# Kernel optimization log

Measured on AMD Instinct MI355X. Metric: run time of the kernel, lower is better.

The kernel has to match this reference:

```python
import jax, jax.numpy as jnp
import numpy as np

DM = 1024
N_HEADS = 16
DK = DM // N_HEADS
BS, SEQ = 4, 2048


def setup_inputs() -> dict:
    key = jax.random.key(0)
    k1, k2, k3 = jax.random.split(key, 3)
    scale = 1.0 / np.sqrt(DM)
    return {
        "x": jax.random.normal(k1, (BS, SEQ, DM), dtype=jnp.float32),
        "w_qkv": jax.random.normal(k2, (DM, 3 * DM), dtype=jnp.float32) * scale,
        "b_qkv": jnp.zeros((3 * DM,), dtype=jnp.float32),
        "w_out": jax.random.normal(k3, (DM, DM), dtype=jnp.float32) * scale,
        "b_out": jnp.zeros((DM,), dtype=jnp.float32),
    }


def reference(x, w_qkv, b_qkv, w_out, b_out):
    bs, seq_len, dm = x.shape
    qkv = x @ w_qkv + b_qkv                      # [bs, seq, 3*dm]
    q, k, v = jnp.split(qkv, 3, axis=-1)
    # [bs, heads, seq, dk]
    def heads(t):
        return t.reshape(bs, seq_len, N_HEADS, DK).transpose(0, 2, 1, 3)
    q, k, v = heads(q), heads(k), heads(v)
    w = jnp.einsum("bhqd,bhkd->bhqk", q, k) / np.sqrt(DK)
    causal = jnp.tril(jnp.ones((seq_len, seq_len), dtype=bool))
    w = jnp.where(causal, w, -jnp.inf)
    w = jax.nn.softmax(w, axis=-1)               # attn_dropout p=0 -> identity
    z = jnp.einsum("bhqk,bhkd->bhqd", w, v)
    z = z.transpose(0, 2, 1, 3).reshape(bs, seq_len, dm)
    return z @ w_out + b_out                     # resid_dropout p=0 -> identity
```

## Files before the change

kernel.cpp:

```cpp
#include <hip/hip_runtime.h>
#include <hip/hip_bf16.h>

typedef unsigned short u16;
typedef unsigned int u32;
typedef short bf16x8 __attribute__((ext_vector_type(8)));
typedef float f32x4 __attribute__((ext_vector_type(4)));

#define DM 1024
#define SEQ 2048
#define MTOK 8192
#define NQKV 3072

#define QSCALE 0.18033688011112042f

#define BAR() __builtin_amdgcn_s_barrier()
#define VMW(n) asm volatile("s_waitcnt vmcnt(" #n ")" ::: "memory")
#define LGKW() asm volatile("s_waitcnt lgkmcnt(0)" ::: "memory")

__device__ __forceinline__ u16 f2bf(float f) {
  union { float f; unsigned u; } a; a.f = f;
  unsigned r = a.u + 0x7FFFu + ((a.u >> 16) & 1u);
  return (u16)(r >> 16);
}

__device__ __forceinline__ u32 cvt2(float a, float b) {
  __hip_bfloat162 t = __float22bfloat162_rn(make_float2(a, b));
  u32 r; __builtin_memcpy(&r, &t, 4); return r;
}

__device__ __forceinline__ void gload_lds16(const u16* g, u16* l) {
  __builtin_amdgcn_global_load_lds(
      (const __attribute__((address_space(1))) unsigned int*)g,
      (__attribute__((address_space(3))) unsigned int*)l, 16, 0, 0);
}

__global__ __launch_bounds__(256) void cast_x_kernel(const float* __restrict__ in,
                                                     u16* __restrict__ out) {
  int i = blockIdx.x * 256 + threadIdx.x;
  float4 v = ((const float4*)in)[i];
  ushort4 o;
  o.x = f2bf(v.x); o.y = f2bf(v.y); o.z = f2bf(v.z); o.w = f2bf(v.w);
  ((ushort4*)out)[i] = o;
}

__global__ __launch_bounds__(256) void transpose_cast_kernel(const float* __restrict__ in,
                                                             u16* __restrict__ out,
                                                             int R, int C) {
  __shared__ float tile[32][33];
  const int tx = threadIdx.x & 31, ty = threadIdx.x >> 5;
  const int r0 = blockIdx.y << 5, c0 = blockIdx.x << 5;
#pragma unroll
  for (int i = 0; i < 32; i += 8)
    tile[ty + i][tx] = in[(size_t)(r0 + ty + i) * C + (c0 + tx)];
  __syncthreads();
#pragma unroll
  for (int i = 0; i < 32; i += 8)
    out[(size_t)(c0 + ty + i) * R + (r0 + tx)] = f2bf(tile[tx][ty + i]);
}

template <int EPI>
__global__ __launch_bounds__(256, 2) void gemm2_kernel(
    const u16* __restrict__ A, const u16* __restrict__ Bt,
    const float* __restrict__ bias,
    u16* __restrict__ oq, u16* __restrict__ ok, u16* __restrict__ ovT,
    float* __restrict__ of, int N) {
  __shared__ alignas(16) u16 As[2][128 * 64];
  __shared__ alignas(16) u16 Bs[2][128 * 64];

  const int tid = threadIdx.x, lane = tid & 63, wid = tid >> 6;
  const int wr = wid >> 1, wc = wid & 1;
  const int l15 = lane & 15, l4 = lane >> 4;
  const int swz = l15 & 7;

  const int xcd = blockIdx.x & 7, idx = blockIdx.x >> 3;
  const int row0 = ((xcd << 3) + (idx & 7)) << 7;
  const int col0 = (idx >> 3) << 7;

  const int sr = tid >> 3;
  const int scsw = ((tid & 7) ^ (sr & 7)) << 3;
  const u16* asrc = A + (size_t)(row0 + sr) * 1024 + scsw;
  const u16* bsrc = Bt + (size_t)(col0 + sr) * 1024 + scsw;

  auto stage = [&](int buf, int kt) {
#pragma unroll
    for (int j = 0; j < 4; ++j)
      gload_lds16(asrc + (size_t)(j << 5) * 1024 + (kt << 6),
                  &As[buf][0] + (j << 11) + tid * 8);
#pragma unroll
    for (int j = 0; j < 4; ++j)
      gload_lds16(bsrc + (size_t)(j << 5) * 1024 + (kt << 6),
                  &Bs[buf][0] + (j << 11) + tid * 8);
  };

  f32x4 acc[4][4];
#pragma unroll
  for (int m = 0; m < 4; ++m)
#pragma unroll
    for (int n = 0; n < 4; ++n) acc[m][n] = (f32x4){0.f, 0.f, 0.f, 0.f};

  stage(0, 0);
  stage(1, 1);

  int cur = 0;
#pragma unroll 1
  for (int t = 0; t < 16; ++t) {
    if (t < 15) { VMW(8); } else { VMW(0); }
    BAR();

    bf16x8 af[4][2], bfr[4][2];
    {
      const u16* base = &As[cur][0] + ((wr << 6) + l15) * 64;
#pragma unroll
      for (int mf = 0; mf < 4; ++mf)
#pragma unroll
        for (int ks = 0; ks < 2; ++ks)
          af[mf][ks] = *(const bf16x8*)(base + (mf << 4) * 64 + ((((ks << 2) + l4) ^ swz) << 3));
    }
    {
      const u16* base = &Bs[cur][0] + ((wc << 6) + l15) * 64;
#pragma unroll
      for (int nf = 0; nf < 4; ++nf)
#pragma unroll
        for (int ks = 0; ks < 2; ++ks)
          bfr[nf][ks] = *(const bf16x8*)(base + (nf << 4) * 64 + ((((ks << 2) + l4) ^ swz) << 3));
    }
    LGKW();
    BAR();
    if (t < 14) stage(cur, t + 2);

    __builtin_amdgcn_s_setprio(1);
#pragma unroll
    for (int ks = 0; ks < 2; ++ks)
#pragma unroll
      for (int mf = 0; mf < 4; ++mf)
#pragma unroll
        for (int nf = 0; nf < 4; ++nf)
          acc[mf][nf] = __builtin_amdgcn_mfma_f32_16x16x32_bf16(af[mf][ks], bfr[nf][ks],
                                                                acc[mf][nf], 0, 0, 0);
    __builtin_amdgcn_s_setprio(0);
    cur ^= 1;
  }

#pragma unroll
  for (int nf = 0; nf < 4; ++nf) {
    const int col = col0 + (wc << 6) + (nf << 4) + l15;
    const float bv = bias[col];
    if (EPI == 0) {
      const int sel = col >> 10;
      const int h = (col & 1023) >> 6;
      const int d = col & 63;
      const float scl = (sel == 0) ? QSCALE : 1.0f;
#pragma unroll
      for (int mf = 0; mf < 4; ++mf)
#pragma unroll
        for (int r = 0; r < 4; ++r) {
          const int row = row0 + (wr << 6) + (mf << 4) + (l4 << 2) + r;
          const int bb = row >> 11, s = row & 2047;
          const u16 v = f2bf((acc[mf][nf][r] + bv) * scl);
          const int bh = (bb << 4) + h;
          if (sel == 0)      oq[((size_t)bh * SEQ + s) * 64 + d] = v;
          else if (sel == 1) ok[((size_t)bh * SEQ + s) * 64 + d] = v;
          else               ovT[((size_t)bh * 64 + d) * SEQ + s] = v;
        }
    } else {
#pragma unroll
      for (int mf = 0; mf < 4; ++mf)
#pragma unroll
        for (int r = 0; r < 4; ++r) {
          const int row = row0 + (wr << 6) + (mf << 4) + (l4 << 2) + r;
          of[(size_t)row * N + col] = acc[mf][nf][r] + bv;
        }
    }
  }
}

__global__ __launch_bounds__(256, 4) void attn_kernel(const u16* __restrict__ qb,
                                                      const u16* __restrict__ kbuf,
                                                      const u16* __restrict__ vT,
                                                      u16* __restrict__ zb) {
  __shared__ alignas(16) u16 Ks[2][64 * 64];
  __shared__ alignas(16) u16 Vs[2][64 * 64];
  __shared__ alignas(16) u16 Ps[4][16 * 64];

  const int bid = blockIdx.x;
  const int xcd = bid & 7;
  const int idx = bid >> 3;
  const int bh = (xcd << 3) | (idx & 7);
  const int qpart = idx >> 3;
  const u32 qtab[4] = {0x0304080Fu, 0x0205090Eu, 0x01060A0Du, 0x00070B0Cu};
  const int qseg = (int)((qtab[qpart & 3] >> ((qpart >> 2) << 3)) & 15u);
  const int b = bh >> 4, h = bh & 15;

  const int tid = threadIdx.x;
  const int lane = tid & 63, wid = tid >> 6;
  const int l15 = lane & 15, l4 = lane >> 4;
  const int swz = l15 & 7;

  const u16* qp = qb + (size_t)bh * SEQ * 64;
  const u16* kp = kbuf + (size_t)bh * SEQ * 64;
  const u16* vp = vT + (size_t)bh * 64 * SEQ;

  const int qw0 = (qseg << 7) + (wid << 5);
  const int nkt = (qseg + 1) << 1;
  const int ktmax = (qseg << 1) + (wid >> 1);

  const int srow = tid >> 3;
  const int schk = ((tid & 7) ^ (srow & 7)) << 3;
  const u16* ksrc = kp + (size_t)srow * 64 + schk;
  const u16* vsrc = vp + (size_t)srow * SEQ + schk;

  auto stage = [&](int buf, int kt) {
    gload_lds16(ksrc + (size_t)kt * 4096, &Ks[buf][0] + tid * 8);
    gload_lds16(ksrc + (size_t)kt * 4096 + 32 * 64, &Ks[buf][0] + 2048 + tid * 8);
    gload_lds16(vsrc + (size_t)kt * 64, &Vs[buf][0] + tid * 8);
    gload_lds16(vsrc + (size_t)kt * 64 + (size_t)32 * SEQ, &Vs[buf][0] + 2048 + tid * 8);
  };

  bf16x8 aq[2][2];
#pragma unroll
  for (int m = 0; m < 2; ++m)
#pragma unroll
    for (int c = 0; c < 2; ++c)
      aq[m][c] = *(const bf16x8*)(qp + (size_t)(qw0 + (m << 4) + l15) * 64 + (c << 5) + (l4 << 3));
  asm volatile("" :: "v"(aq[0][0]), "v"(aq[0][1]), "v"(aq[1][0]), "v"(aq[1][1]));

  const short osv = (short)0x3F80;
  const bf16x8 onesf = {osv, osv, osv, osv, osv, osv, osv, osv};

  f32x4 zo[2][5];
  float mrun[2] = {-INFINITY, -INFINITY};
#pragma unroll
  for (int m = 0; m < 2; ++m)
#pragma unroll
    for (int d = 0; d < 5; ++d) zo[m][d] = (f32x4){0.f, 0.f, 0.f, 0.f};

  u16* pw = &Ps[wid][0];

  stage(0, 0);
  stage(1, 1);

  int cur = 0;
#pragma unroll 1
  for (int kt = 0; kt < nkt; ++kt) {
    if (kt + 1 < nkt) { VMW(4); } else { VMW(0); }
    BAR();

    if (kt <= ktmax) {
      const int k0 = kt << 6;
      const u16* kb_ = &Ks[cur][0];
      const u16* vb_ = &Vs[cur][0];
      f32x4 s[2][4];
#pragma unroll
      for (int m = 0; m < 2; ++m)
#pragma unroll
        for (int nf = 0; nf < 4; ++nf) s[m][nf] = (f32x4){0.f, 0.f, 0.f, 0.f};
#pragma unroll
      for (int nf = 0; nf < 4; ++nf) {
        const u16* kr = kb_ + ((nf << 4) + l15) * 64;
        const bf16x8 kf0 = *(const bf16x8*)(kr + ((l4 ^ swz) << 3));
        const bf16x8 kf1 = *(const bf16x8*)(kr + (((l4 + 4) ^ swz) << 3));
#pragma unroll
        for (int m = 0; m < 2; ++m) {
          s[m][nf] = __builtin_amdgcn_mfma_f32_16x16x32_bf16(kf0, aq[m][0], s[m][nf], 0, 0, 0);
          s[m][nf] = __builtin_amdgcn_mfma_f32_16x16x32_bf16(kf1, aq[m][1], s[m][nf], 0, 0, 0);
        }
      }
      if (kt == ktmax) {
#pragma unroll
        for (int m = 0; m < 2; ++m) {
          const int qtok = qw0 + (m << 4) + l15;
#pragma unroll
          for (int nf = 0; nf < 4; ++nf)
#pragma unroll
            for (int r = 0; r < 4; ++r) {
              const int ktok = k0 + (nf << 4) + (l4 << 2) + r;
              if (ktok > qtok) s[m][nf][r] = -INFINITY;
            }
        }
      }
      bf16x8 pa[2][2];
#pragma unroll
      for (int m = 0; m < 2; ++m) {
        float mx = s[m][0][0];
#pragma unroll
        for (int nf = 0; nf < 4; ++nf)
#pragma unroll
          for (int r = 0; r < 4; ++r) mx = fmaxf(mx, s[m][nf][r]);
        mx = fmaxf(mx, __shfl_xor(mx, 16));
        mx = fmaxf(mx, __shfl_xor(mx, 32));
        if (__ballot(mx > mrun[m])) {
          const float mnew = fmaxf(mrun[m], mx);
          const float alpha = exp2f(mrun[m] - mnew);
          mrun[m] = mnew;
#pragma unroll
          for (int d = 0; d < 5; ++d) zo[m][d] *= alpha;
        }
#pragma unroll
        for (int nf = 0; nf < 4; ++nf) {
          f32x4 p;
#pragma unroll
          for (int r = 0; r < 4; ++r) p[r] = exp2f(s[m][nf][r] - mrun[m]);
          const int phys = ((nf << 1) + (l4 >> 1)) ^ swz;
          uint2 o; o.x = cvt2(p[0], p[1]); o.y = cvt2(p[2], p[3]);
          *(uint2*)(pw + l15 * 64 + phys * 8 + ((l4 & 1) << 2)) = o;
        }
#pragma unroll
        for (int c = 0; c < 2; ++c) {
          const int phys = ((c << 2) + l4) ^ swz;
          pa[m][c] = *(const bf16x8*)(pw + l15 * 64 + phys * 8);
        }
      }
#pragma unroll
      for (int d = 0; d < 4; ++d) {
        const u16* vr = vb_ + ((d << 4) + l15) * 64;
        const bf16x8 vf0 = *(const bf16x8*)(vr + ((l4 ^ swz) << 3));
        const bf16x8 vf1 = *(const bf16x8*)(vr + (((l4 + 4) ^ swz) << 3));
        zo[0][d] = __builtin_amdgcn_mfma_f32_16x16x32_bf16(vf0, pa[0][0], zo[0][d], 0, 0, 0);
        zo[0][d] = __builtin_amdgcn_mfma_f32_16x16x32_bf16(vf1, pa[0][1], zo[0][d], 0, 0, 0);
        zo[1][d] = __builtin_amdgcn_mfma_f32_16x16x32_bf16(vf0, pa[1][0], zo[1][d], 0, 0, 0);
        zo[1][d] = __builtin_amdgcn_mfma_f32_16x16x32_bf16(vf1, pa[1][1], zo[1][d], 0, 0, 0);
      }
      zo[0][4] = __builtin_amdgcn_mfma_f32_16x16x32_bf16(onesf, pa[0][0], zo[0][4], 0, 0, 0);
      zo[0][4] = __builtin_amdgcn_mfma_f32_16x16x32_bf16(onesf, pa[0][1], zo[0][4], 0, 0, 0);
      zo[1][4] = __builtin_amdgcn_mfma_f32_16x16x32_bf16(onesf, pa[1][0], zo[1][4], 0, 0, 0);
      zo[1][4] = __builtin_amdgcn_mfma_f32_16x16x32_bf16(onesf, pa[1][1], zo[1][4], 0, 0, 0);
    }

    BAR();
    if (kt + 2 < nkt) stage(cur, kt + 2);
    cur ^= 1;
  }

#pragma unroll
  for (int m = 0; m < 2; ++m) {
    const float inv = 1.0f / zo[m][4][0];
    const int q = qw0 + (m << 4) + l15;
#pragma unroll
    for (int d = 0; d < 4; ++d) {
      uint2 o;
      o.x = cvt2(zo[m][d][0] * inv, zo[m][d][1] * inv);
      o.y = cvt2(zo[m][d][2] * inv, zo[m][d][3] * inv);
      *(uint2*)(zb + (((size_t)b * SEQ + q) * 16 + h) * 64 + (d << 4) + (l4 << 2)) = o;
    }
  }
}

extern "C" void kernel_launch(void* const* d_in, const int* in_sizes, int n_in,
                              void* d_out, int out_size, void* d_ws, size_t ws_size,
                              hipStream_t stream) {
  const float* x     = (const float*)d_in[0];
  const float* w_qkv = (const float*)d_in[1];
  const float* b_qkv = (const float*)d_in[2];
  const float* w_out = (const float*)d_in[3];
  const float* b_out = (const float*)d_in[4];
  float* out = (float*)d_out;

  char* ws = (char*)d_ws;
  u16* xb    = (u16*)ws;  ws += (size_t)MTOK * DM * 2;
  u16* wqkvT = (u16*)ws;  ws += (size_t)NQKV * DM * 2;
  u16* woutT = (u16*)ws;  ws += (size_t)DM * DM * 2;
  u16* qb    = (u16*)ws;  ws += (size_t)MTOK * DM * 2;
  u16* kb    = (u16*)ws;  ws += (size_t)MTOK * DM * 2;
  u16* vTb   = (u16*)ws;  ws += (size_t)MTOK * DM * 2;
  u16* zbuf  = (u16*)ws;  ws += (size_t)MTOK * DM * 2;

  cast_x_kernel<<<MTOK * DM / 1024, 256, 0, stream>>>(x, xb);
  transpose_cast_kernel<<<dim3(NQKV / 32, DM / 32), 256, 0, stream>>>(w_qkv, wqkvT, DM, NQKV);
  transpose_cast_kernel<<<dim3(DM / 32, DM / 32), 256, 0, stream>>>(w_out, woutT, DM, DM);

  gemm2_kernel<0><<<1536, 256, 0, stream>>>(xb, wqkvT, b_qkv, qb, kb, vTb, nullptr, NQKV);

  attn_kernel<<<1024, 256, 0, stream>>>(qb, kb, vTb, zbuf);

  gemm2_kernel<1><<<512, 256, 0, stream>>>(zbuf, woutT, b_out, nullptr, nullptr, nullptr, out, DM);
}
```

Measured before the change: 192.3 us.

## Add 256x256-tile 8-wave QKV GEMM with split-stage pipelined loads

Replaces the 128x128-tile QKV projection GEMM with a dedicated 512-thread kernel that computes 256x256 tiles, one block per CU. Each K step loads its tile in two halves interleaved with four quadrant MFMA phases, so global-to-LDS staging overlaps compute. The larger tile raises arithmetic intensity and cuts redundant global loads. In exchange it uses 128KB of LDS and 128 accumulator registers per thread, and the grid shrinks to 384 blocks, which risks wave-quantization imbalance across CUs. The output GEMM is de-templated, with no functional change.

```diff
diff --git a/kernel.cpp b/kernel.cpp
--- a/kernel.cpp
+++ b/kernel.cpp
@@ -58,12 +58,128 @@
     out[(size_t)(c0 + ty + i) * R + (r0 + tx)] = f2bf(tile[tx][ty + i]);
 }
 
-template <int EPI>
+__global__ __launch_bounds__(512, 1) void gemm8_qkv_kernel(
+    const u16* __restrict__ A, const u16* __restrict__ Bt,
+    const float* __restrict__ bias,
+    u16* __restrict__ oq, u16* __restrict__ ok, u16* __restrict__ ovT) {
+  __shared__ alignas(16) u16 As8[2][256 * 64];
+  __shared__ alignas(16) u16 Bs8[2][256 * 64];
+
+  const int tid = threadIdx.x, lane = tid & 63, wid = tid >> 6;
+  const int wm = wid >> 2, wn = wid & 3;
+  const int l15 = lane & 15, l4 = lane >> 4;
+  const int swz = l15 & 7;
+
+  const int bid = blockIdx.x;
+  const int xcd = bid & 7, i = bid >> 3;
+  const int brow = (xcd << 2) + (i & 3);
+  const int bcol = i >> 2;
+  const int row0 = brow << 8, col0 = bcol << 8;
+
+  const int sr = tid >> 3;
+  const int sc = tid & 7;
+
+  auto stageU = [&](int buf, int kt, int half) {
+#pragma unroll
+    for (int j = 0; j < 2; ++j) {
+      const int r = (half << 7) + (j << 6) + sr;
+      gload_lds16(Bt + (size_t)(col0 + r) * 1024 + (kt << 6) + ((sc ^ (r & 7)) << 3),
+                  &Bs8[buf][0] + r * 64 + (sc << 3));
+    }
+#pragma unroll
+    for (int j = 0; j < 2; ++j) {
+      const int r = (half << 7) + (j << 6) + sr;
+      gload_lds16(A + (size_t)(row0 + r) * 1024 + (kt << 6) + ((sc ^ (r & 7)) << 3),
+                  &As8[buf][0] + r * 64 + (sc << 3));
+    }
+  };
+
+  f32x4 acc[8][4];
+#pragma unroll
+  for (int m = 0; m < 8; ++m)
+#pragma unroll
+    for (int n = 0; n < 4; ++n) acc[m][n] = (f32x4){0.f, 0.f, 0.f, 0.f};
+
+  bf16x8 af[4][2], bf0[2][2], bf1[2][2];
+
+  auto rdA = [&](int buf, int mh) {
+    const u16* base = &As8[buf][0] + ((wm << 7) + (mh << 6) + l15) * 64;
+#pragma unroll
+    for (int mf = 0; mf < 4; ++mf)
+#pragma unroll
+      for (int ks = 0; ks < 2; ++ks)
+        af[mf][ks] = *(const bf16x8*)(base + (mf << 4) * 64 + ((((ks << 2) + l4) ^ swz) << 3));
+  };
+  auto rdB = [&](bf16x8 (&bf)[2][2], int buf, int nh) {
+    const u16* base = &Bs8[buf][0] + ((wn << 6) + (nh << 5) + l15) * 64;
+#pragma unroll
+    for (int nfl = 0; nfl < 2; ++nfl)
+#pragma unroll
+      for (int ks = 0; ks < 2; ++ks)
+        bf[nfl][ks] = *(const bf16x8*)(base + (nfl << 4) * 64 + ((((ks << 2) + l4) ^ swz) << 3));
+  };
+  auto mm = [&](bf16x8 (&bf)[2][2], int mh, int nh) {
+    __builtin_amdgcn_s_setprio(1);
+#pragma unroll
+    for (int mf = 0; mf < 4; ++mf)
+#pragma unroll
+      for (int nfl = 0; nfl < 2; ++nfl)
+#pragma unroll
+        for (int ks = 0; ks < 2; ++ks)
+          acc[(mh << 2) + mf][(nh << 1) + nfl] = __builtin_amdgcn_mfma_f32_16x16x32_bf16(
+              af[mf][ks], bf[nfl][ks], acc[(mh << 2) + mf][(nh << 1) + nfl], 0, 0, 0);
+    __builtin_amdgcn_s_setprio(0);
+  };
+
+  stageU(0, 0, 0);
+  stageU(0, 0, 1);
+
+#pragma unroll 1
+  for (int t = 0; t < 16; ++t) {
+    const int buf = t & 1, nbuf = buf ^ 1;
+    if (t < 15) { stageU(nbuf, t + 1, 0); VMW(4); } else { VMW(0); }
+    BAR();
+    rdA(buf, 0); rdB(bf0, buf, 0);
+    mm(bf0, 0, 0);
+    BAR();
+    if (t < 15) stageU(nbuf, t + 1, 1);
+    BAR();
+    rdB(bf1, buf, 1);
+    mm(bf1, 0, 1);
+    BAR();
+    rdA(buf, 1);
+    mm(bf0, 1, 0);
+    BAR();
+    mm(bf1, 1, 1);
+    BAR();
+  }
+
+#pragma unroll
+  for (int nf = 0; nf < 4; ++nf) {
+    const int col = col0 + (wn << 6) + (nf << 4) + l15;
+    const float bv = bias[col];
+    const int sel = col >> 10;
+    const int hh = (col & 1023) >> 6;
+    const int d = col & 63;
+    const float scl = (sel == 0) ? QSCALE : 1.0f;
+#pragma unroll
+    for (int mf = 0; mf < 8; ++mf)
+#pragma unroll
+      for (int r = 0; r < 4; ++r) {
+        const int row = row0 + (wm << 7) + (mf << 4) + (l4 << 2) + r;
+        const int bb = row >> 11, s = row & 2047;
+        const u16 v = f2bf((acc[mf][nf][r] + bv) * scl);
+        const int bh = (bb << 4) + hh;
+        if (sel == 0)      oq[((size_t)bh * SEQ + s) * 64 + d] = v;
+        else if (sel == 1) ok[((size_t)bh * SEQ + s) * 64 + d] = v;
+        else               ovT[((size_t)bh * 64 + d) * SEQ + s] = v;
+      }
+  }
+}
+
 __global__ __launch_bounds__(256, 2) void gemm2_kernel(
     const u16* __restrict__ A, const u16* __restrict__ Bt,
-    const float* __restrict__ bias,
-    u16* __restrict__ oq, u16* __restrict__ ok, u16* __restrict__ ovT,
-    float* __restrict__ of, int N) {
+    const float* __restrict__ bias, float* __restrict__ of, int N) {
   __shared__ alignas(16) u16 As[2][128 * 64];
   __shared__ alignas(16) u16 Bs[2][128 * 64];
 
@@ -145,32 +261,13 @@
   for (int nf = 0; nf < 4; ++nf) {
     const int col = col0 + (wc << 6) + (nf << 4) + l15;
     const float bv = bias[col];
-    if (EPI == 0) {
-      const int sel = col >> 10;
-      const int h = (col & 1023) >> 6;
-      const int d = col & 63;
-      const float scl = (sel == 0) ? QSCALE : 1.0f;
-#pragma unroll
-      for (int mf = 0; mf < 4; ++mf)
-#pragma unroll
-        for (int r = 0; r < 4; ++r) {
-          const int row = row0 + (wr << 6) + (mf << 4) + (l4 << 2) + r;
-          const int bb = row >> 11, s = row & 2047;
-          const u16 v = f2bf((acc[mf][nf][r] + bv) * scl);
-          const int bh = (bb << 4) + h;
-          if (sel == 0)      oq[((size_t)bh * SEQ + s) * 64 + d] = v;
-          else if (sel == 1) ok[((size_t)bh * SEQ + s) * 64 + d] = v;
-          else               ovT[((size_t)bh * 64 + d) * SEQ + s] = v;
-        }
-    } else {
-#pragma unroll
-      for (int mf = 0; mf < 4; ++mf)
-#pragma unroll
-        for (int r = 0; r < 4; ++r) {
-          const int row = row0 + (wr << 6) + (mf << 4) + (l4 << 2) + r;
-          of[(size_t)row * N + col] = acc[mf][nf][r] + bv;
-        }
-    }
+#pragma unroll
+    for (int mf = 0; mf < 4; ++mf)
+#pragma unroll
+      for (int r = 0; r < 4; ++r) {
+        const int row = row0 + (wr << 6) + (mf << 4) + (l4 << 2) + r;
+        of[(size_t)row * N + col] = acc[mf][nf][r] + bv;
+      }
   }
 }
 
@@ -368,9 +465,9 @@
   transpose_cast_kernel<<<dim3(NQKV / 32, DM / 32), 256, 0, stream>>>(w_qkv, wqkvT, DM, NQKV);
   transpose_cast_kernel<<<dim3(DM / 32, DM / 32), 256, 0, stream>>>(w_out, woutT, DM, DM);
 
-  gemm2_kernel<0><<<1536, 256, 0, stream>>>(xb, wqkvT, b_qkv, qb, kb, vTb, nullptr, NQKV);
+  gemm8_qkv_kernel<<<384, 512, 0, stream>>>(xb, wqkvT, b_qkv, qb, kb, vTb);
 
   attn_kernel<<<1024, 256, 0, stream>>>(qb, kb, vTb, zbuf);
 
-  gemm2_kernel<1><<<512, 256, 0, stream>>>(zbuf, woutT, b_out, nullptr, nullptr, nullptr, out, DM);
-}
+  gemm2_kernel<<<512, 256, 0, stream>>>(zbuf, woutT, b_out, out, DM);
+}
```

After: 220.0 us. 14.4% more time.
